# Optimization experiments

Hardware: AMD Instinct MI355X
Metric: run time of the kernel (lower is better)

The kernel has to match this reference:

```python
import jax, jax.numpy as jnp
import numpy as np

N, E, G = 50000, 800000, 16
H, C = 4, 64  # heads, per-head channels
NEG_SLOPE = 0.2

def gat_conv(x, src, dst, W, att_s, att_d, bias, heads, out_c, concat):
    # x: [N, Fin]; W: [Fin, heads*out_c]; att_s/att_d: [heads, out_c]
    h = (x @ W).reshape(N, heads, out_c)
    a_s = (h * att_s).sum(-1)              # [N, heads]
    a_d = (h * att_d).sum(-1)
    e = a_s[src] + a_d[dst]                # [E, heads]
    e = jnp.where(e >= 0, e, NEG_SLOPE * e)  # leaky_relu
    m = jax.ops.segment_max(e, dst, num_segments=N)
    ex = jnp.exp(e - m[dst])
    den = jax.ops.segment_sum(ex, dst, num_segments=N)
    alpha = ex / (den[dst] + 1e-16)        # segment softmax over incoming edges
    msg = h[src] * alpha[:, :, None]       # [E, heads, out_c]
    out = jax.ops.segment_sum(msg, dst, num_segments=N)
    out = out.reshape(N, heads * out_c) if concat else out.mean(axis=1)
    return out + bias

def setup_inputs() -> dict:
    key = jax.random.key(0)
    ks = jax.random.split(key, 30)
    def g(k, shape, scale=0.05):
        return (jax.random.normal(k, shape, dtype=jnp.float32) * scale)
    inp = {}
    inp['x'] = jax.random.normal(ks[0], (N, 32), dtype=jnp.float32)
    inp['edge_index'] = jax.random.randint(ks[1], (2, E), 0, N, dtype=jnp.int32)
    inp['batch'] = jnp.sort(jax.random.randint(ks[2], (N,), 0, G, dtype=jnp.int32))
    inp['global_features'] = jax.random.normal(ks[3], (G, 4), dtype=jnp.float32)
    # node encoder
    inp['W_enc'] = g(ks[4], (32, C)); inp['b_enc'] = g(ks[5], (C,))
    # conv1: 64 -> 4x64 concat
    inp['W1'] = g(ks[6], (C, H * C)); inp['as1'] = g(ks[7], (H, C)); inp['ad1'] = g(ks[8], (H, C)); inp['b1'] = g(ks[9], (H * C,))
    # conv2: 256 -> 4x64 concat
    inp['W2'] = g(ks[10], (H * C, H * C)); inp['as2'] = g(ks[11], (H, C)); inp['ad2'] = g(ks[12], (H, C)); inp['b2'] = g(ks[13], (H * C,))
    # conv3: 256 -> 1x64 no concat
    inp['W3'] = g(ks[14], (H * C, C)); inp['as3'] = g(ks[15], (1, C)); inp['ad3'] = g(ks[16], (1, C)); inp['b3'] = g(ks[17], (C,))
    # global processor
    inp['Wg'] = g(ks[18], (4, C)); inp['bg'] = g(ks[19], (C,))
    # decoder
    inp['Wd1'] = g(ks[20], (2 * C, C)); inp['bd1'] = g(ks[21], (C,))
    inp['gamma'] = jnp.ones((C,), jnp.float32); inp['beta'] = jnp.zeros((C,), jnp.float32)
    inp['Wd2'] = g(ks[22], (C, 256)); inp['bd2'] = g(ks[23], (256,))
    return inp

def reference(x, edge_index, batch, global_features, W_enc, b_enc,
              W1, as1, ad1, b1, W2, as2, ad2, b2, W3, as3, ad3, b3,
              Wg, bg, Wd1, bd1, gamma, beta, Wd2, bd2):
    # add self-loops (PyG GATConv default)
    loops = jnp.arange(N, dtype=edge_index.dtype)
    src = jnp.concatenate([edge_index[0], loops])
    dst = jnp.concatenate([edge_index[1], loops])
    h = x @ W_enc + b_enc
    h = gat_conv(h, src, dst, W1, as1, ad1, b1, H, C, True)
    h = jax.nn.elu(h)  # dropout is identity in eval
    h = gat_conv(h, src, dst, W2, as2, ad2, b2, H, C, True)
    h = jax.nn.elu(h)
    h = gat_conv(h, src, dst, W3, as3, ad3, b3, 1, C, False)
    # global mean pool per graph
    sums = jax.ops.segment_sum(h, batch, num_segments=G)
    cnts = jax.ops.segment_sum(jnp.ones((N, 1), h.dtype), batch, num_segments=G)
    pooled = sums / jnp.maximum(cnts, 1.0)
    genc = jax.nn.relu(global_features @ Wg + bg)
    z = jnp.concatenate([pooled, genc], axis=1)
    z = z @ Wd1 + bd1
    z = z * gamma + beta  # BatchNorm1d in eval mode (running stats 0/1)
    z = jax.nn.relu(z)
    out = z @ Wd2 + bd2
    return jax.nn.softmax(out, axis=1)
```

## Files before the change

kernel.cpp:

```cpp
#include <hip/hip_runtime.h>
#include <math.h>

#define NEG_SLOPE 0.2f
#define LOG2E 1.4426950408889634f

typedef __attribute__((ext_vector_type(8))) short short8;
typedef __attribute__((ext_vector_type(4))) float f32x4;

__device__ inline float b2f(unsigned short u) {
    union { unsigned int i; float f; } x; x.i = ((unsigned int)u) << 16; return x.f;
}
__device__ inline float b2f_lo(unsigned int u) {
    union { unsigned int i; float f; } x; x.i = u << 16; return x.f;
}
__device__ inline float b2f_hi(unsigned int u) {
    union { unsigned int i; float f; } x; x.i = u & 0xFFFF0000u; return x.f;
}
__device__ inline unsigned short f2b(float f) {
    union { float f; unsigned int i; } u; u.f = f;
    unsigned int r = u.i + 0x7FFF + ((u.i >> 16) & 1);
    return (unsigned short)(r >> 16);
}

__global__ void prep_kernel(const float* __restrict__ W1, const float* __restrict__ W2,
                            const float* __restrict__ W3, const float* __restrict__ as1,
                            const float* __restrict__ ad1,
                            unsigned short* __restrict__ Wt1, unsigned short* __restrict__ Wt2,
                            unsigned short* __restrict__ Wt3,
                            float* __restrict__ u1s, float* __restrict__ u1d,
                            int* __restrict__ counts, float* __restrict__ pooledP,
                            float* __restrict__ cntP, int N, int G, int zc) {
    const int b = blockIdx.x;
    const int t = threadIdx.x;
    if (b < 64) {
        int i = b * 256 + t;
        int k = i >> 8, m = i & 255;
        Wt1[(size_t)m * 64 + k] = f2b(W1[i]);
    } else if (b < 320) {
        int i = (b - 64) * 256 + t;
        int k = i >> 8, m = i & 255;
        Wt2[(size_t)m * 256 + k] = f2b(W2[i]);
    } else if (b < 384) {
        int i = (b - 320) * 256 + t;
        int k = i >> 6, m = i & 63;
        Wt3[(size_t)m * 256 + k] = f2b(W3[i]);
    } else if (b == 384) {
        int k = t >> 2, h = t & 3;
        float s = 0.0f, d = 0.0f;
        for (int c = 0; c < 64; c++) {
            float w = W1[k * 256 + h * 64 + c];
            s += w * as1[h * 64 + c];
            d += w * ad1[h * 64 + c];
        }
        u1s[k * 4 + h] = s;
        u1d[k * 4 + h] = d;
    } else if (b < 385 + zc) {
        int i = (b - 385) * 256 + t;
        if (i < N) counts[i] = 0;
    } else {
        int i = (b - 385 - zc) * 256 + t;
        if (i < 64 * G * 64) pooledP[i] = 0.0f;
        if (i < 64 * G) cntP[i] = 0.0f;
    }
}

__global__ __launch_bounds__(256) void gemm_enc(const float* __restrict__ A,
                                                const float* __restrict__ B,
                                                const float* __restrict__ bias,
                                                unsigned short* __restrict__ C16,
                                                const float* __restrict__ u1s,
                                                const float* __restrict__ u1d,
                                                float* __restrict__ a_s,
                                                float* __restrict__ a_d,
                                                int Nrows, int K, int M) {
    __shared__ float sA[16][64];
    __shared__ float sB[16][64];
    const int tx = threadIdx.x & 15;
    const int ty = threadIdx.x >> 4;
    const int row0 = blockIdx.x * 64;
    const int lr = threadIdx.x >> 2;
    const int lk = (threadIdx.x & 3) << 2;
    const int br = threadIdx.x >> 4;
    const int bc = (threadIdx.x & 15) << 2;

    const int aRow = row0 + lr;
    const bool aValid = aRow < Nrows;
    const float* Aptr = A + (size_t)aRow * K + lk;
    const float* Bptr = B + (size_t)br * M + bc;

    float acc[4][4] = {{0,0,0,0},{0,0,0,0},{0,0,0,0},{0,0,0,0}};
    float4 a = aValid ? *(const float4*)Aptr : float4{0,0,0,0};
    float4 b = *(const float4*)Bptr;

    for (int kt = 0; kt < K; kt += 16) {
        __syncthreads();
        sA[lk+0][lr] = a.x; sA[lk+1][lr] = a.y; sA[lk+2][lr] = a.z; sA[lk+3][lr] = a.w;
        *(float4*)&sB[br][bc] = b;
        __syncthreads();
        if (kt + 16 < K) {
            a = aValid ? *(const float4*)(Aptr + kt + 16) : float4{0,0,0,0};
            b = *(const float4*)(Bptr + (size_t)(kt + 16) * M);
        }
        #pragma unroll
        for (int k = 0; k < 16; k++) {
            const float4 av = *(const float4*)&sA[k][ty << 2];
            const float4 bv = *(const float4*)&sB[k][tx << 2];
            acc[0][0] += av.x*bv.x; acc[0][1] += av.x*bv.y; acc[0][2] += av.x*bv.z; acc[0][3] += av.x*bv.w;
            acc[1][0] += av.y*bv.x; acc[1][1] += av.y*bv.y; acc[1][2] += av.y*bv.z; acc[1][3] += av.y*bv.w;
            acc[2][0] += av.z*bv.x; acc[2][1] += av.z*bv.y; acc[2][2] += av.z*bv.z; acc[2][3] += av.z*bv.w;
            acc[3][0] += av.w*bv.x; acc[3][1] += av.w*bv.y; acc[3][2] += av.w*bv.z; acc[3][3] += av.w*bv.w;
        }
    }
    float4 bb = *(const float4*)&bias[tx << 2];
    #pragma unroll
    for (int i = 0; i < 4; i++) {
        acc[i][0] += bb.x; acc[i][1] += bb.y; acc[i][2] += bb.z; acc[i][3] += bb.w;
    }
    float4 us[4], ud[4];
    #pragma unroll
    for (int j = 0; j < 4; j++) {
        us[j] = *(const float4*)&u1s[((tx << 2) + j) * 4];
        ud[j] = *(const float4*)&u1d[((tx << 2) + j) * 4];
    }
    #pragma unroll
    for (int i = 0; i < 4; i++) {
        float4 ps = {0,0,0,0}, pd = {0,0,0,0};
        #pragma unroll
        for (int j = 0; j < 4; j++) {
            ps.x += acc[i][j] * us[j].x; ps.y += acc[i][j] * us[j].y;
            ps.z += acc[i][j] * us[j].z; ps.w += acc[i][j] * us[j].w;
            pd.x += acc[i][j] * ud[j].x; pd.y += acc[i][j] * ud[j].y;
            pd.z += acc[i][j] * ud[j].z; pd.w += acc[i][j] * ud[j].w;
        }
        #pragma unroll
        for (int off = 1; off < 16; off <<= 1) {
            ps.x += __shfl_xor(ps.x, off); ps.y += __shfl_xor(ps.y, off);
            ps.z += __shfl_xor(ps.z, off); ps.w += __shfl_xor(ps.w, off);
            pd.x += __shfl_xor(pd.x, off); pd.y += __shfl_xor(pd.y, off);
            pd.z += __shfl_xor(pd.z, off); pd.w += __shfl_xor(pd.w, off);
        }
        int r = row0 + (ty << 2) + i;
        if (tx == 0 && r < Nrows) {
            float4 o1 = {ps.x * LOG2E, ps.y * LOG2E, ps.z * LOG2E, ps.w * LOG2E};
            float4 o2 = {pd.x * LOG2E, pd.y * LOG2E, pd.z * LOG2E, pd.w * LOG2E};
            *(float4*)&a_s[r * 4] = o1;
            *(float4*)&a_d[r * 4] = o2;
        }
    }
    #pragma unroll
    for (int i = 0; i < 4; i++) {
        int r = row0 + (ty << 2) + i;
        if (r < Nrows) {
            ushort4 o = {f2b(acc[i][0]), f2b(acc[i][1]), f2b(acc[i][2]), f2b(acc[i][3])};
            *(ushort4*)&C16[(size_t)r * M + (tx << 2)] = o;
        }
    }
}

template<int CPW, int SCORES>
__global__ __launch_bounds__(256) void gemm_mfma(const unsigned short* __restrict__ A16,
                                                 const unsigned short* __restrict__ Bt16,
                                                 unsigned short* __restrict__ C16,
                                                 const float* __restrict__ att_s,
                                                 const float* __restrict__ att_d,
                                                 float* __restrict__ a_s,
                                                 float* __restrict__ a_d,
                                                 int Nrows, int K, int M, int H) {
    constexpr int BN = CPW * 64;
    __shared__ unsigned short sA[64][40];
    __shared__ unsigned short sB[BN][40];
    const int tid = threadIdx.x;
    const int wave = tid >> 6;
    const int lane = tid & 63;
    const int quad = lane >> 4;
    const int l16 = lane & 15;
    const int row0 = blockIdx.x * 64;
    const int col0 = blockIdx.y * BN;
    const int sr = tid >> 2;
    const int sk = (tid & 3) << 3;

    f32x4 acc[4][CPW];
    #pragma unroll
    for (int i = 0; i < 4; i++)
        #pragma unroll
        for (int j = 0; j < CPW; j++) acc[i][j] = (f32x4){0,0,0,0};

    for (int kt = 0; kt < K; kt += 32) {
        __syncthreads();
// ... 52 lines not shown
            if (l16 == 0) {
                #pragma unroll
                for (int r = 0; r < 4; r++) {
                    atomicAdd(&sSD[i * 16 + quad * 4 + r][hib][0], ps[r]);
                    atomicAdd(&sSD[i * 16 + quad * 4 + r][hib][1], pd[r]);
                }
            }
        }
        __syncthreads();
        for (int t = tid; t < 64 * CPW; t += 256) {
            int row = t & 63, hb = t >> 6;
            int r = row0 + row;
            if (r < Nrows) {
                int hg = (col0 >> 6) + hb;
                a_s[r * H + hg] = sSD[row][hb][0] * LOG2E;
                a_d[r * H + hg] = sSD[row][hb][1] * LOG2E;
            }
        }
    }
    #pragma unroll
    for (int i = 0; i < 4; i++) {
        #pragma unroll
        for (int j = 0; j < CPW; j++) {
            int col = col0 + wave * (CPW * 16) + j * 16 + l16;
            #pragma unroll
            for (int r = 0; r < 4; r++) {
                int row = row0 + i * 16 + quad * 4 + r;
                if (row < Nrows) C16[(size_t)row * M + col] = f2b(acc[i][j][r]);
            }
        }
    }
}

__global__ __launch_bounds__(256) void gemm_bd64(const unsigned short* __restrict__ A16,
                                                 const unsigned short* __restrict__ Bt16,
                                                 const float* __restrict__ bias,
                                                 unsigned short* __restrict__ C16,
                                                 int Nrows) {
    __shared__ unsigned short sA[64][40];
    __shared__ unsigned short sB[64][40];
    const int tid = threadIdx.x;
    const int wave = tid >> 6;
    const int lane = tid & 63;
    const int quad = lane >> 4;
    const int l16 = lane & 15;
    const int h = blockIdx.y;
    const int row0 = blockIdx.x * 64;
    const int sr = tid >> 2;
    const int sk = (tid & 3) << 3;

    f32x4 acc[4];
    #pragma unroll
    for (int i = 0; i < 4; i++) acc[i] = (f32x4){0,0,0,0};

    #pragma unroll
    for (int kt = 0; kt < 64; kt += 32) {
        __syncthreads();
        {
            int r = row0 + sr;
            uint4 z = {0,0,0,0};
            *(uint4*)&sA[sr][sk] = (r < Nrows)
                ? *(const uint4*)&A16[(size_t)r * 256 + h * 64 + kt + sk] : z;
        }
        *(uint4*)&sB[sr][sk] = *(const uint4*)&Bt16[(size_t)(h * 64 + sr) * 64 + kt + sk];
        __syncthreads();
        short8 bf = *(const short8*)&sB[wave * 16 + l16][quad * 8];
        #pragma unroll
        for (int i = 0; i < 4; i++) {
            short8 af = *(const short8*)&sA[i * 16 + l16][quad * 8];
            acc[i] = __builtin_amdgcn_mfma_f32_16x16x32_bf16(af, bf, acc[i], 0, 0, 0);
        }
    }
    const int col = h * 64 + wave * 16 + l16;
    const float bb = bias[col];
    #pragma unroll
    for (int i = 0; i < 4; i++) {
        #pragma unroll
        for (int r = 0; r < 4; r++) {
            int row = row0 + i * 16 + quad * 4 + r;
            if (row < Nrows) {
                float v = acc[i][r] + bb;
                v = (v > 0.0f) ? v : expm1f(v);
                C16[(size_t)row * 256 + col] = f2b(v);
            }
        }
    }
}

__global__ void edge_hist_kernel(const int* __restrict__ ei, int* __restrict__ counts,
                                 int E, int Et) {
    int e = blockIdx.x * 256 + threadIdx.x;
    if (e >= Et) return;
    int d = (e < E) ? ei[E + e] : e - E;
    atomicAdd(&counts[d], 1);
}

__global__ __launch_bounds__(1024) void scan_blocks(int* __restrict__ counts,
                                                    int* __restrict__ blockSums, int N) {
    __shared__ int wsum[16];
    const int tid = threadIdx.x;
    const int lane = tid & 63;
    const int wave = tid >> 6;
    int i = blockIdx.x * 1024 + tid;
    int v = (i < N) ? counts[i] : 0;
// ... 26 lines not shown
                          int N, int Et) {
    __shared__ int sbs[64];
    if (threadIdx.x < 64) {
        int lane = threadIdx.x;
        int v = (lane < nb) ? blockSums[lane] : 0;
        int s = v;
        #pragma unroll
        for (int off = 1; off < 64; off <<= 1) {
            int t = __shfl_up(s, off);
            if (lane >= off) s += t;
        }
        sbs[lane] = s - v;
    }
    __syncthreads();
    int i = blockIdx.x * 256 + threadIdx.x;
    if (i < N) {
        int o = excl[i] + sbs[i >> 10];
        offsets[i] = o;
        cursor[i] = o;
    }
    if (i == N) offsets[N] = Et;
}

__global__ void edge_sort_kernel(const int* __restrict__ ei, int* __restrict__ cursor,
                                 int* __restrict__ srcS, int E, int Et) {
    int e = blockIdx.x * 256 + threadIdx.x;
    if (e >= Et) return;
    int s, d;
    if (e < E) { s = ei[e]; d = ei[E + e]; } else { s = d = e - E; }
    int pos = atomicAdd(&cursor[d], 1);
    srcS[pos] = s;
}

__global__ __launch_bounds__(256) void gat_agg_in64(
        const int* __restrict__ offsets, const int* __restrict__ srcS,
        const float4* __restrict__ a_s4, const float4* __restrict__ a_d4,
        const unsigned short* __restrict__ h16,
        unsigned short* __restrict__ out16,
        int N) {
    __shared__ float wlds[4][64][4];
    __shared__ int slds[4][64];
    const int wid = threadIdx.x >> 6;
    const int n = blockIdx.x * 4 + wid;
    if (n >= N) return;
    const int lane = threadIdx.x & 63;
    const int half = lane >> 5;
    const int l32 = lane & 31;
    const int start = offsets[n], end = offsets[n + 1];
    const float4 ad = a_d4[n];
    float2 acc[4] = {{0,0},{0,0},{0,0},{0,0}};
    float4 den = {0,0,0,0};
    const int loff = l32 << 1;

    for (int e0 = start; e0 < end; e0 += 64) {
        const int cnt = min(64, end - e0);
        if (lane < cnt) {
            int sB = srcS[e0 + lane];
            slds[wid][lane] = sB;
            const float4 as = a_s4[sB];
            float x0 = as.x + ad.x; x0 = fmaxf(x0, NEG_SLOPE * x0);
            float x1 = as.y + ad.y; x1 = fmaxf(x1, NEG_SLOPE * x1);
            float x2 = as.z + ad.z; x2 = fmaxf(x2, NEG_SLOPE * x2);
            float x3 = as.w + ad.w; x3 = fmaxf(x3, NEG_SLOPE * x3);
            wlds[wid][lane][0] = exp2f(x0);
            wlds[wid][lane][1] = exp2f(x1);
            wlds[wid][lane][2] = exp2f(x2);
            wlds[wid][lane][3] = exp2f(x3);
        }
        int j = half;
        for (; j + 8 <= cnt + half; j += 8) {
            int ss[4]; float4 ww[4]; unsigned int gg[4];
            #pragma unroll
            for (int u = 0; u < 4; u++) {
                ss[u] = slds[wid][j + 2 * u];
                ww[u] = *(const float4*)&wlds[wid][j + 2 * u][0];
            }
            #pragma unroll
            for (int u = 0; u < 4; u++)
                gg[u] = *(const unsigned int*)&h16[((size_t)ss[u] << 6) + loff];
            #pragma unroll
            for (int u = 0; u < 4; u++) {
                const float vl = b2f_lo(gg[u]), vh = b2f_hi(gg[u]);
                acc[0].x += ww[u].x * vl; acc[0].y += ww[u].x * vh;
                acc[1].x += ww[u].y * vl; acc[1].y += ww[u].y * vh;
                acc[2].x += ww[u].z * vl; acc[2].y += ww[u].z * vh;
                acc[3].x += ww[u].w * vl; acc[3].y += ww[u].w * vh;
                den.x += ww[u].x; den.y += ww[u].y; den.z += ww[u].z; den.w += ww[u].w;
            }
        }
        for (; j < cnt; j += 2) {
            const int s = slds[wid][j];
            const float4 w = *(const float4*)&wlds[wid][j][0];
            const unsigned int g = *(const unsigned int*)&h16[((size_t)s << 6) + loff];
            const float vl = b2f_lo(g), vh = b2f_hi(g);
            acc[0].x += w.x * vl; acc[0].y += w.x * vh;
            acc[1].x += w.y * vl; acc[1].y += w.y * vh;
            acc[2].x += w.z * vl; acc[2].y += w.z * vh;
            acc[3].x += w.w * vl; acc[3].y += w.w * vh;
            den.x += w.x; den.y += w.y; den.z += w.z; den.w += w.w;
        }
    }
    #pragma unroll
    for (int h = 0; h < 4; h++) {
        acc[h].x += __shfl_xor(acc[h].x, 32);
        acc[h].y += __shfl_xor(acc[h].y, 32);
    }
    den.x += __shfl_xor(den.x, 32); den.y += __shfl_xor(den.y, 32);
    den.z += __shfl_xor(den.z, 32); den.w += __shfl_xor(den.w, 32);
    if (half == 0) {
        const float i0 = 1.0f / (den.x + 1e-16f);
        const float i1 = 1.0f / (den.y + 1e-16f);
        const float i2 = 1.0f / (den.z + 1e-16f);
        const float i3 = 1.0f / (den.w + 1e-16f);
        unsigned int o0 = (unsigned int)f2b(acc[0].x * i0) | ((unsigned int)f2b(acc[0].y * i0) << 16);
        unsigned int o1 = (unsigned int)f2b(acc[1].x * i1) | ((unsigned int)f2b(acc[1].y * i1) << 16);
        unsigned int o2 = (unsigned int)f2b(acc[2].x * i2) | ((unsigned int)f2b(acc[2].y * i2) << 16);
        unsigned int o3 = (unsigned int)f2b(acc[3].x * i3) | ((unsigned int)f2b(acc[3].y * i3) << 16);
        *(unsigned int*)&out16[(size_t)n * 256 + 0 * 64 + loff] = o0;
        *(unsigned int*)&out16[(size_t)n * 256 + 1 * 64 + loff] = o1;
        *(unsigned int*)&out16[(size_t)n * 256 + 2 * 64 + loff] = o2;
        *(unsigned int*)&out16[(size_t)n * 256 + 3 * 64 + loff] = o3;
    }
}

__global__ __launch_bounds__(256) void gat_fused4(
        const int* __restrict__ offsets, const int* __restrict__ srcS,
        const float4* __restrict__ a_s4, const float4* __restrict__ a_d4,
        const unsigned short* __restrict__ hW16, const float* __restrict__ bias,
        unsigned short* __restrict__ out16, int N) {
    __shared__ float wlds[4][64][4];
    __shared__ int slds[4][64];
    const int wid = threadIdx.x >> 6;
    const int n = blockIdx.x * 4 + wid;
    if (n >= N) return;
    const int lane = threadIdx.x & 63;
    const int quad = lane >> 4;
    const int start = offsets[n], end = offsets[n + 1];
    const float4 ad = a_d4[n];
    float4 acc = {0, 0, 0, 0};
    float den = 0.0f;
    const int loff = lane << 2;

    for (int e0 = start; e0 < end; e0 += 64) {
        const int cnt = min(64, end - e0);
        if (lane < cnt) {
            int sB = srcS[e0 + lane];
            slds[wid][lane] = sB;
            const float4 as = a_s4[sB];
            float x0 = as.x + ad.x; x0 = fmaxf(x0, NEG_SLOPE * x0);
            float x1 = as.y + ad.y; x1 = fmaxf(x1, NEG_SLOPE * x1);
            float x2 = as.z + ad.z; x2 = fmaxf(x2, NEG_SLOPE * x2);
            float x3 = as.w + ad.w; x3 = fmaxf(x3, NEG_SLOPE * x3);
            wlds[wid][lane][0] = exp2f(x0);
            wlds[wid][lane][1] = exp2f(x1);
            wlds[wid][lane][2] = exp2f(x2);
            wlds[wid][lane][3] = exp2f(x3);
        }
        int j = 0;
        for (; j + 4 <= cnt; j += 4) {
            const int s0 = __builtin_amdgcn_readfirstlane(slds[wid][j + 0]);
            const int s1 = __builtin_amdgcn_readfirstlane(slds[wid][j + 1]);
            const int s2 = __builtin_amdgcn_readfirstlane(slds[wid][j + 2]);
            const int s3 = __builtin_amdgcn_readfirstlane(slds[wid][j + 3]);
            const float w0 = wlds[wid][j + 0][quad];
            const float w1 = wlds[wid][j + 1][quad];
            const float w2 = wlds[wid][j + 2][quad];
            const float w3 = wlds[wid][j + 3][quad];
            const uint2 h0 = *(const uint2*)&hW16[((size_t)s0 << 8) + loff];
            const uint2 h1 = *(const uint2*)&hW16[((size_t)s1 << 8) + loff];
            const uint2 h2 = *(const uint2*)&hW16[((size_t)s2 << 8) + loff];
            const uint2 h3 = *(const uint2*)&hW16[((size_t)s3 << 8) + loff];
            acc.x += w0 * b2f_lo(h0.x); acc.y += w0 * b2f_hi(h0.x);
            acc.z += w0 * b2f_lo(h0.y); acc.w += w0 * b2f_hi(h0.y);
            acc.x += w1 * b2f_lo(h1.x); acc.y += w1 * b2f_hi(h1.x);
            acc.z += w1 * b2f_lo(h1.y); acc.w += w1 * b2f_hi(h1.y);
            acc.x += w2 * b2f_lo(h2.x); acc.y += w2 * b2f_hi(h2.x);
            acc.z += w2 * b2f_lo(h2.y); acc.w += w2 * b2f_hi(h2.y);
            acc.x += w3 * b2f_lo(h3.x); acc.y += w3 * b2f_hi(h3.x);
            acc.z += w3 * b2f_lo(h3.y); acc.w += w3 * b2f_hi(h3.y);
            den += (w0 + w1) + (w2 + w3);
        }
        for (; j < cnt; j++) {
            const int s = __builtin_amdgcn_readfirstlane(slds[wid][j]);
            const float w = wlds[wid][j][quad];
            const uint2 hv = *(const uint2*)&hW16[((size_t)s << 8) + loff];
            acc.x += w * b2f_lo(hv.x); acc.y += w * b2f_hi(hv.x);
            acc.z += w * b2f_lo(hv.y); acc.w += w * b2f_hi(hv.y);
            den += w;
        }
    }

    const float inv = 1.0f / (den + 1e-16f);
    const float4 bb = *(const float4*)&bias[loff];
    float v0 = acc.x * inv + bb.x; v0 = (v0 > 0.0f) ? v0 : expm1f(v0);
    float v1 = acc.y * inv + bb.y; v1 = (v1 > 0.0f) ? v1 : expm1f(v1);
    float v2 = acc.z * inv + bb.z; v2 = (v2 > 0.0f) ? v2 : expm1f(v2);
    float v3 = acc.w * inv + bb.w; v3 = (v3 > 0.0f) ? v3 : expm1f(v3);
    uint2 o;
    o.x = (unsigned int)f2b(v0) | ((unsigned int)f2b(v1) << 16);
    o.y = (unsigned int)f2b(v2) | ((unsigned int)f2b(v3) << 16);
    *(uint2*)&out16[(size_t)n * 256 + loff] = o;
}

__global__ __launch_bounds__(256) void gat_fused1(
        const int* __restrict__ offsets, const int* __restrict__ srcS,
        const float* __restrict__ a_s, const float* __restrict__ a_d,
        const unsigned short* __restrict__ hW16, const float* __restrict__ bias,
        const int* __restrict__ batch,
        float* __restrict__ pooledP, float* __restrict__ cntP, int N, int G) {
    __shared__ float wlds[4][64];
    __shared__ int slds[4][64];
    __shared__ float2 sOut[4][32];
    __shared__ int sG[4];
    const int wid = threadIdx.x >> 6;
    const int n = blockIdx.x * 4 + wid;
    const bool valid = n < N;
    const int lane = threadIdx.x & 63;
    const int half = lane >> 5;
    const int l32 = lane & 31;
    const int start = valid ? offsets[n] : 0;
    const int end   = valid ? offsets[n + 1] : 0;
    const float ad  = valid ? a_d[n] : 0.0f;
    float accx = 0.0f, accy = 0.0f, den = 0.0f;
    const int loff = l32 << 1;

    for (int e0 = start; e0 < end; e0 += 64) {
        const int cnt_ = min(64, end - e0);
        if (lane < cnt_) {
            int sB = srcS[e0 + lane];
            slds[wid][lane] = sB;
            float ev = a_s[sB] + ad;
            ev = fmaxf(ev, NEG_SLOPE * ev);
            wlds[wid][lane] = exp2f(ev);
        }
// ... 144 lines not shown
    const int*   batch = (const int*)  d_in[2];
    const float* gf    = (const float*)d_in[3];
    const float* W_enc = (const float*)d_in[4];
    const float* b_enc = (const float*)d_in[5];
    const float* W1  = (const float*)d_in[6];
    const float* as1 = (const float*)d_in[7];
    const float* ad1 = (const float*)d_in[8];
    const float* b1  = (const float*)d_in[9];
    const float* W2  = (const float*)d_in[10];
    const float* as2 = (const float*)d_in[11];
    const float* ad2 = (const float*)d_in[12];
    const float* b2  = (const float*)d_in[13];
    const float* W3  = (const float*)d_in[14];
    const float* as3 = (const float*)d_in[15];
    const float* ad3 = (const float*)d_in[16];
    const float* b3  = (const float*)d_in[17];
    const float* Wg  = (const float*)d_in[18];
    const float* bg  = (const float*)d_in[19];
    const float* Wd1 = (const float*)d_in[20];
    const float* bd1 = (const float*)d_in[21];
    const float* gm  = (const float*)d_in[22];
    const float* bt  = (const float*)d_in[23];
    const float* Wd2 = (const float*)d_in[24];
    const float* bd2 = (const float*)d_in[25];

    const int N  = in_sizes[2];
    const int E  = in_sizes[1] / 2;
    const int G  = in_sizes[3] / 4;
    const int Et = E + N;

    unsigned short* h16a = (unsigned short*)d_ws;
    unsigned short* h16b = h16a + (size_t)N * 256;
    unsigned short* h1_16 = h16b + (size_t)N * 256;
    unsigned short* Wt1  = h1_16 + (size_t)N * 64;
    unsigned short* Wt2  = Wt1 + 256 * 64;
    unsigned short* Wt3  = Wt2 + 256 * 256;
    float* a_s    = (float*)(Wt3 + 64 * 256);
    float* a_d    = a_s + (size_t)N * 4;
    float* u1s    = a_d + (size_t)N * 4;
    float* u1d    = u1s + 256;
    float* pooledP = u1d + 256;
    float* cntP   = pooledP + (size_t)64 * G * 64;
    int*   offsets = (int*)(cntP + 64 * G);
    int*   srcS    = offsets + (N + 1);
    int*   counts  = srcS + Et;
    int*   cursor  = counts + N;
    int*   blockSums = cursor + N;

    dim3 blk(256);
    auto cdiv = [](int a, int b) { return (a + b - 1) / b; };
    const int eBlocks = cdiv(Et, 256);
    const int rowBlocks = cdiv(N, 64);
    const int nScanBlocks = cdiv(N, 1024);
    const int zc = cdiv(N, 256);
    const int z2 = cdiv(64 * G * 64, 256);

    prep_kernel<<<385 + zc + z2, blk, 0, stream>>>(W1, W2, W3, as1, ad1, Wt1, Wt2, Wt3,
                                                   u1s, u1d, counts, pooledP, cntP, N, G, zc);
    edge_hist_kernel<<<eBlocks, blk, 0, stream>>>(ei, counts, E, Et);
    scan_blocks<<<nScanBlocks, 1024, 0, stream>>>(counts, blockSums, N);
    scan_add2<<<cdiv(N + 1, 256), blk, 0, stream>>>(counts, blockSums, nScanBlocks,
                                                    offsets, cursor, N, Et);
    edge_sort_kernel<<<eBlocks, blk, 0, stream>>>(ei, cursor, srcS, E, Et);

    gemm_enc<<<dim3(rowBlocks, 1), blk, 0, stream>>>(x, W_enc, b_enc, h1_16,
                                                     u1s, u1d, a_s, a_d, N, 32, 64);

    gat_agg_in64<<<cdiv(N, 4), blk, 0, stream>>>(offsets, srcS, (const float4*)a_s,
                                                 (const float4*)a_d, h1_16, h16a, N);
    gemm_bd64<<<dim3(rowBlocks, 4), blk, 0, stream>>>(h16a, Wt1, b1, h16b, N);

    gemm_mfma<2, 1><<<dim3(rowBlocks, 2), blk, 0, stream>>>(h16b, Wt2, h16a,
                                                            as2, ad2, a_s, a_d, N, 256, 256, 4);
    gat_fused4<<<cdiv(N, 4), blk, 0, stream>>>(offsets, srcS, (const float4*)a_s,
                                               (const float4*)a_d, h16a, b2, h16b, N);

    gemm_mfma<1, 1><<<dim3(rowBlocks, 1), blk, 0, stream>>>(h16b, Wt3, h1_16,
                                                            as3, ad3, a_s, a_d, N, 256, 64, 1);
    gat_fused1<<<cdiv(N, 4), blk, 0, stream>>>(offsets, srcS, a_s, a_d, h1_16, b3,
                                               batch, pooledP, cntP, N, G);

    final_kernel<<<G, blk, 0, stream>>>(pooledP, cntP, gf, Wg, bg, Wd1, bd1, gm, bt, Wd2, bd2,
                                        (float*)d_out, G);
}
```

Before: 429.6 us.

## Split layer-2 GAT aggregation across heads via grid y dimension

The 4-head aggregation kernel now launches one wave per (node, head) using a second grid dimension. Each wave handles a single 64-channel head slice, with two half-waves processing alternating edges and combining results by a cross-lane shuffle. This raises parallelism and memory-level concurrency for the gather. The cost is that srcS and a_s are re-read and exp weights recomputed once per head, and each gather is narrower (4 bytes per lane instead of 8).

```diff
diff --git a/kernel.cpp b/kernel.cpp
--- a/kernel.cpp
+++ b/kernel.cpp
@@ -493,83 +493,78 @@
     }
 }
 
-__global__ __launch_bounds__(256) void gat_fused4(
+__global__ __launch_bounds__(256) void gat_fused4h(
         const int* __restrict__ offsets, const int* __restrict__ srcS,
-        const float4* __restrict__ a_s4, const float4* __restrict__ a_d4,
-        const unsigned short* __restrict__ hW16, const float* __restrict__ bias,
-        unsigned short* __restrict__ out16, int N) {
-    __shared__ float wlds[4][64][4];
+        const float* __restrict__ a_s,
+        const float* __restrict__ a_d,
+        const unsigned short* __restrict__ hW16,
+        const float* __restrict__ bias,
+        unsigned short* __restrict__ out16,
+        int N) {
+    __shared__ float wlds[4][64];
     __shared__ int slds[4][64];
     const int wid = threadIdx.x >> 6;
     const int n = blockIdx.x * 4 + wid;
     if (n >= N) return;
+    const int h = blockIdx.y;
     const int lane = threadIdx.x & 63;
-    const int quad = lane >> 4;
+    const int half = lane >> 5;
+    const int l32 = lane & 31;
     const int start = offsets[n], end = offsets[n + 1];
-    const float4 ad = a_d4[n];
-    float4 acc = {0, 0, 0, 0};
-    float den = 0.0f;
-    const int loff = lane << 2;
+    const float ad = a_d[n * 4 + h];
+    float accx = 0.0f, accy = 0.0f, den = 0.0f;
+    const int loff = l32 << 1;
+    const size_t colbase = (size_t)h * 64 + loff;
 
     for (int e0 = start; e0 < end; e0 += 64) {
-        const int cnt = min(64, end - e0);
-        if (lane < cnt) {
+        const int cnt_ = min(64, end - e0);
+        if (lane < cnt_) {
             int sB = srcS[e0 + lane];
             slds[wid][lane] = sB;
-            const float4 as = a_s4[sB];
-            float x0 = as.x + ad.x; x0 = fmaxf(x0, NEG_SLOPE * x0);
-            float x1 = as.y + ad.y; x1 = fmaxf(x1, NEG_SLOPE * x1);
-            float x2 = as.z + ad.z; x2 = fmaxf(x2, NEG_SLOPE * x2);
-            float x3 = as.w + ad.w; x3 = fmaxf(x3, NEG_SLOPE * x3);
-            wlds[wid][lane][0] = exp2f(x0);
-            wlds[wid][lane][1] = exp2f(x1);
-            wlds[wid][lane][2] = exp2f(x2);
-            wlds[wid][lane][3] = exp2f(x3);
-        }
-        int j = 0;
-        for (; j + 4 <= cnt; j += 4) {
-            const int s0 = __builtin_amdgcn_readfirstlane(slds[wid][j + 0]);
-            const int s1 = __builtin_amdgcn_readfirstlane(slds[wid][j + 1]);
-            const int s2 = __builtin_amdgcn_readfirstlane(slds[wid][j + 2]);
-            const int s3 = __builtin_amdgcn_readfirstlane(slds[wid][j + 3]);
-            const float w0 = wlds[wid][j + 0][quad];
-            const float w1 = wlds[wid][j + 1][quad];
-            const float w2 = wlds[wid][j + 2][quad];
-            const float w3 = wlds[wid][j + 3][quad];
-            const uint2 h0 = *(const uint2*)&hW16[((size_t)s0 << 8) + loff];
-            const uint2 h1 = *(const uint2*)&hW16[((size_t)s1 << 8) + loff];
-            const uint2 h2 = *(const uint2*)&hW16[((size_t)s2 << 8) + loff];
-            const uint2 h3 = *(const uint2*)&hW16[((size_t)s3 << 8) + loff];
-            acc.x += w0 * b2f_lo(h0.x); acc.y += w0 * b2f_hi(h0.x);
-            acc.z += w0 * b2f_lo(h0.y); acc.w += w0 * b2f_hi(h0.y);
-            acc.x += w1 * b2f_lo(h1.x); acc.y += w1 * b2f_hi(h1.x);
-            acc.z += w1 * b2f_lo(h1.y); acc.w += w1 * b2f_hi(h1.y);
-            acc.x += w2 * b2f_lo(h2.x); acc.y += w2 * b2f_hi(h2.x);
-            acc.z += w2 * b2f_lo(h2.y); acc.w += w2 * b2f_hi(h2.y);
-            acc.x += w3 * b2f_lo(h3.x); acc.y += w3 * b2f_hi(h3.x);
-            acc.z += w3 * b2f_lo(h3.y); acc.w += w3 * b2f_hi(h3.y);
+            float ev = a_s[sB * 4 + h] + ad;
+            ev = fmaxf(ev, NEG_SLOPE * ev);
+            wlds[wid][lane] = exp2f(ev);
+        }
+        int j = half;
+        for (; j + 8 <= cnt_ + half; j += 8) {
+            const int s0 = slds[wid][j + 0];
+            const int s1 = slds[wid][j + 2];
+            const int s2 = slds[wid][j + 4];
+            const int s3 = slds[wid][j + 6];
+            const float w0 = wlds[wid][j + 0];
+            const float w1 = wlds[wid][j + 2];
+            const float w2 = wlds[wid][j + 4];
+            const float w3 = wlds[wid][j + 6];
+            const unsigned int h0 = *(const unsigned int*)&hW16[((size_t)s0 << 8) + colbase];
+            const unsigned int h1 = *(const unsigned int*)&hW16[((size_t)s1 << 8) + colbase];
+            const unsigned int h2 = *(const unsigned int*)&hW16[((size_t)s2 << 8) + colbase];
+            const unsigned int h3 = *(const unsigned int*)&hW16[((size_t)s3 << 8) + colbase];
+            accx += w0 * b2f_lo(h0); accy += w0 * b2f_hi(h0);
+            accx += w1 * b2f_lo(h1); accy += w1 * b2f_hi(h1);
+            accx += w2 * b2f_lo(h2); accy += w2 * b2f_hi(h2);
+            accx += w3 * b2f_lo(h3); accy += w3 * b2f_hi(h3);
             den += (w0 + w1) + (w2 + w3);
         }
-        for (; j < cnt; j++) {
-            const int s = __builtin_amdgcn_readfirstlane(slds[wid][j]);
-            const float w = wlds[wid][j][quad];
-            const uint2 hv = *(const uint2*)&hW16[((size_t)s << 8) + loff];
-            acc.x += w * b2f_lo(hv.x); acc.y += w * b2f_hi(hv.x);
-            acc.z += w * b2f_lo(hv.y); acc.w += w * b2f_hi(hv.y);
+        for (; j < cnt_; j += 2) {
+            const int s = slds[wid][j];
+            const float w = wlds[wid][j];
+            const unsigned int hv = *(const unsigned int*)&hW16[((size_t)s << 8) + colbase];
+            accx += w * b2f_lo(hv);
+            accy += w * b2f_hi(hv);
             den += w;
         }
     }
-
-    const float inv = 1.0f / (den + 1e-16f);
-    const float4 bb = *(const float4*)&bias[loff];
-    float v0 = acc.x * inv + bb.x; v0 = (v0 > 0.0f) ? v0 : expm1f(v0);
-    float v1 = acc.y * inv + bb.y; v1 = (v1 > 0.0f) ? v1 : expm1f(v1);
-    float v2 = acc.z * inv + bb.z; v2 = (v2 > 0.0f) ? v2 : expm1f(v2);
-    float v3 = acc.w * inv + bb.w; v3 = (v3 > 0.0f) ? v3 : expm1f(v3);
-    uint2 o;
-    o.x = (unsigned int)f2b(v0) | ((unsigned int)f2b(v1) << 16);
-    o.y = (unsigned int)f2b(v2) | ((unsigned int)f2b(v3) << 16);
-    *(uint2*)&out16[(size_t)n * 256 + loff] = o;
+    accx += __shfl_xor(accx, 32);
+    accy += __shfl_xor(accy, 32);
+    den  += __shfl_xor(den, 32);
+    if (half == 0) {
+        const float inv = 1.0f / (den + 1e-16f);
+        const float2 bb = *(const float2*)&bias[h * 64 + loff];
+        float v0 = accx * inv + bb.x; v0 = (v0 > 0.0f) ? v0 : expm1f(v0);
+        float v1 = accy * inv + bb.y; v1 = (v1 > 0.0f) ? v1 : expm1f(v1);
+        unsigned int o = (unsigned int)f2b(v0) | ((unsigned int)f2b(v1) << 16);
+        *(unsigned int*)&out16[(size_t)n * 256 + h * 64 + loff] = o;
+    }
 }
 
 __global__ __launch_bounds__(256) void gat_fused1(
@@ -820,8 +815,8 @@
 
     gemm_mfma<2, 1><<<dim3(rowBlocks, 2), blk, 0, stream>>>(h16b, Wt2, h16a,
                                                             as2, ad2, a_s, a_d, N, 256, 256, 4);
-    gat_fused4<<<cdiv(N, 4), blk, 0, stream>>>(offsets, srcS, (const float4*)a_s,
-                                               (const float4*)a_d, h16a, b2, h16b, N);
+    gat_fused4h<<<dim3(cdiv(N, 4), 4), blk, 0, stream>>>(offsets, srcS, a_s, a_d,
+                                                         h16a, b2, h16b, N);
 
     gemm_mfma<1, 1><<<dim3(rowBlocks, 1), blk, 0, stream>>>(h16b, Wt3, h1_16,
                                                             as3, ad3, a_s, a_d, N, 256, 64, 1);
```

Result: slower. 461.8 us (+7.5%).

## Fold encoder linear into conv1 weights and aggregate raw 32-dim inputs

Applied to the files above, without the earlier changes.

Because the node encoder is linear, W_enc is folded into W1 (and b_enc into the bias), and attention scores are computed directly from x. Conv1 then aggregates the raw 32-channel bf16 input features per head instead of the 64-channel encoded features, and the per-head GEMM after aggregation uses K=32 instead of 64. This halves the gather bytes in the first aggregation and drops the encoder GEMM, at the cost of an extra 128-wide per-node intermediate and some extra bf16 rounding of the pre-combined weights.

```diff
diff --git a/kernel.cpp b/kernel.cpp
--- a/kernel.cpp
+++ b/kernel.cpp
@@ -7,9 +7,6 @@
 typedef __attribute__((ext_vector_type(8))) short short8;
 typedef __attribute__((ext_vector_type(4))) float f32x4;
 
-__device__ inline float b2f(unsigned short u) {
-    union { unsigned int i; float f; } x; x.i = ((unsigned int)u) << 16; return x.f;
-}
 __device__ inline float b2f_lo(unsigned int u) {
     union { unsigned int i; float f; } x; x.i = u << 16; return x.f;
 }
@@ -22,29 +19,29 @@
     return (unsigned short)(r >> 16);
 }
 
-__global__ void prep_kernel(const float* __restrict__ W1, const float* __restrict__ W2,
+__global__ void prep_kernel(const float* __restrict__ W_enc, const float* __restrict__ b_enc,
+                            const float* __restrict__ W1, const float* __restrict__ W2,
                             const float* __restrict__ W3, const float* __restrict__ as1,
-                            const float* __restrict__ ad1,
-                            unsigned short* __restrict__ Wt1, unsigned short* __restrict__ Wt2,
-                            unsigned short* __restrict__ Wt3,
+                            const float* __restrict__ ad1, const float* __restrict__ b1,
+                            unsigned short* __restrict__ Wc1t, float* __restrict__ bc1,
+                            unsigned short* __restrict__ Wt2, unsigned short* __restrict__ Wt3,
                             float* __restrict__ u1s, float* __restrict__ u1d,
                             int* __restrict__ counts, float* __restrict__ pooledP,
                             float* __restrict__ cntP, int N, int G, int zc) {
     const int b = blockIdx.x;
     const int t = threadIdx.x;
-    if (b < 64) {
+    if (b < 32) {
         int i = b * 256 + t;
-        int k = i >> 8, m = i & 255;
-        Wt1[(size_t)m * 64 + k] = f2b(W1[i]);
-    } else if (b < 320) {
-        int i = (b - 64) * 256 + t;
-        int k = i >> 8, m = i & 255;
-        Wt2[(size_t)m * 256 + k] = f2b(W2[i]);
-    } else if (b < 384) {
-        int i = (b - 320) * 256 + t;
-        int k = i >> 6, m = i & 63;
-        Wt3[(size_t)m * 256 + k] = f2b(W3[i]);
-    } else if (b == 384) {
+        int h = i >> 11, rem = i & 2047, o = rem >> 5, j = rem & 31;
+        float s = 0.0f;
+        for (int k = 0; k < 64; k++)
+            s += W_enc[j * 64 + k] * W1[k * 256 + h * 64 + o];
+        Wc1t[i] = f2b(s);
+    } else if (b == 32) {
+        float s = b1[t];
+        for (int k = 0; k < 64; k++) s += b_enc[k] * W1[k * 256 + t];
+        bc1[t] = s;
+    } else if (b == 33) {
         int k = t >> 2, h = t & 3;
         float s = 0.0f, d = 0.0f;
         for (int c = 0; c < 64; c++) {
@@ -54,106 +51,69 @@
         }
         u1s[k * 4 + h] = s;
         u1d[k * 4 + h] = d;
-    } else if (b < 385 + zc) {
-        int i = (b - 385) * 256 + t;
+    } else if (b < 34 + 256) {
+        int i = (b - 34) * 256 + t;
+        int k = i >> 8, m = i & 255;
+        Wt2[(size_t)m * 256 + k] = f2b(W2[i]);
+    } else if (b < 34 + 256 + 64) {
+        int i = (b - 290) * 256 + t;
+        int k = i >> 6, m = i & 63;
+        Wt3[(size_t)m * 256 + k] = f2b(W3[i]);
+    } else if (b < 354 + zc) {
+        int i = (b - 354) * 256 + t;
         if (i < N) counts[i] = 0;
     } else {
-        int i = (b - 385 - zc) * 256 + t;
+        int i = (b - 354 - zc) * 256 + t;
         if (i < 64 * G * 64) pooledP[i] = 0.0f;
         if (i < 64 * G) cntP[i] = 0.0f;
     }
 }
 
-__global__ __launch_bounds__(256) void gemm_enc(const float* __restrict__ A,
-                                                const float* __restrict__ B,
-                                                const float* __restrict__ bias,
-                                                unsigned short* __restrict__ C16,
-                                                const float* __restrict__ u1s,
-                                                const float* __restrict__ u1d,
-                                                float* __restrict__ a_s,
-                                                float* __restrict__ a_d,
-                                                int Nrows, int K, int M) {
-    __shared__ float sA[16][64];
-    __shared__ float sB[16][64];
-    const int tx = threadIdx.x & 15;
-    const int ty = threadIdx.x >> 4;
-    const int row0 = blockIdx.x * 64;
-    const int lr = threadIdx.x >> 2;
-    const int lk = (threadIdx.x & 3) << 2;
-    const int br = threadIdx.x >> 4;
-    const int bc = (threadIdx.x & 15) << 2;
-
-    const int aRow = row0 + lr;
-    const bool aValid = aRow < Nrows;
-    const float* Aptr = A + (size_t)aRow * K + lk;
-    const float* Bptr = B + (size_t)br * M + bc;
-
-    float acc[4][4] = {{0,0,0,0},{0,0,0,0},{0,0,0,0},{0,0,0,0}};
-    float4 a = aValid ? *(const float4*)Aptr : float4{0,0,0,0};
-    float4 b = *(const float4*)Bptr;
-
-    for (int kt = 0; kt < K; kt += 16) {
-        __syncthreads();
-        sA[lk+0][lr] = a.x; sA[lk+1][lr] = a.y; sA[lk+2][lr] = a.z; sA[lk+3][lr] = a.w;
-        *(float4*)&sB[br][bc] = b;
-        __syncthreads();
-        if (kt + 16 < K) {
-            a = aValid ? *(const float4*)(Aptr + kt + 16) : float4{0,0,0,0};
-            b = *(const float4*)(Bptr + (size_t)(kt + 16) * M);
-        }
-        #pragma unroll
-        for (int k = 0; k < 16; k++) {
-            const float4 av = *(const float4*)&sA[k][ty << 2];
-            const float4 bv = *(const float4*)&sB[k][tx << 2];
-            acc[0][0] += av.x*bv.x; acc[0][1] += av.x*bv.y; acc[0][2] += av.x*bv.z; acc[0][3] += av.x*bv.w;
-            acc[1][0] += av.y*bv.x; acc[1][1] += av.y*bv.y; acc[1][2] += av.y*bv.z; acc[1][3] += av.y*bv.w;
-            acc[2][0] += av.z*bv.x; acc[2][1] += av.z*bv.y; acc[2][2] += av.z*bv.z; acc[2][3] += av.z*bv.w;
-            acc[3][0] += av.w*bv.x; acc[3][1] += av.w*bv.y; acc[3][2] += av.w*bv.z; acc[3][3] += av.w*bv.w;
-        }
-    }
-    float4 bb = *(const float4*)&bias[tx << 2];
-    #pragma unroll
-    for (int i = 0; i < 4; i++) {
-        acc[i][0] += bb.x; acc[i][1] += bb.y; acc[i][2] += bb.z; acc[i][3] += bb.w;
-    }
-    float4 us[4], ud[4];
-    #pragma unroll
-    for (int j = 0; j < 4; j++) {
-        us[j] = *(const float4*)&u1s[((tx << 2) + j) * 4];
-        ud[j] = *(const float4*)&u1d[((tx << 2) + j) * 4];
-    }
-    #pragma unroll
-    for (int i = 0; i < 4; i++) {
-        float4 ps = {0,0,0,0}, pd = {0,0,0,0};
-        #pragma unroll
-        for (int j = 0; j < 4; j++) {
-            ps.x += acc[i][j] * us[j].x; ps.y += acc[i][j] * us[j].y;
-            ps.z += acc[i][j] * us[j].z; ps.w += acc[i][j] * us[j].w;
-            pd.x += acc[i][j] * ud[j].x; pd.y += acc[i][j] * ud[j].y;
-            pd.z += acc[i][j] * ud[j].z; pd.w += acc[i][j] * ud[j].w;
-        }
-        #pragma unroll
-        for (int off = 1; off < 16; off <<= 1) {
-            ps.x += __shfl_xor(ps.x, off); ps.y += __shfl_xor(ps.y, off);
-            ps.z += __shfl_xor(ps.z, off); ps.w += __shfl_xor(ps.w, off);
-            pd.x += __shfl_xor(pd.x, off); pd.y += __shfl_xor(pd.y, off);
-            pd.z += __shfl_xor(pd.z, off); pd.w += __shfl_xor(pd.w, off);
-        }
-        int r = row0 + (ty << 2) + i;
-        if (tx == 0 && r < Nrows) {
-            float4 o1 = {ps.x * LOG2E, ps.y * LOG2E, ps.z * LOG2E, ps.w * LOG2E};
-            float4 o2 = {pd.x * LOG2E, pd.y * LOG2E, pd.z * LOG2E, pd.w * LOG2E};
-            *(float4*)&a_s[r * 4] = o1;
-            *(float4*)&a_d[r * 4] = o2;
-        }
-    }
-    #pragma unroll
-    for (int i = 0; i < 4; i++) {
-        int r = row0 + (ty << 2) + i;
-        if (r < Nrows) {
-            ushort4 o = {f2b(acc[i][0]), f2b(acc[i][1]), f2b(acc[i][2]), f2b(acc[i][3])};
-            *(ushort4*)&C16[(size_t)r * M + (tx << 2)] = o;
-        }
+__global__ __launch_bounds__(256) void score_x(
+        const float* __restrict__ x, const float* __restrict__ W_enc,
+        const float* __restrict__ b_enc,
+        const float* __restrict__ u1s, const float* __restrict__ u1d,
+        unsigned short* __restrict__ x16, float* __restrict__ a_s,
+        float* __restrict__ a_d, int N) {
+    __shared__ float sUs[32][4], sUd[32][4], sC[8];
+    __shared__ float sX[32][33];
+    const int t = threadIdx.x;
+    if (t < 128) {
+        int j = t >> 2, h = t & 3;
+        float s = 0.0f, d = 0.0f;
+        for (int k = 0; k < 64; k++) {
+            float w = W_enc[j * 64 + k];
+            s += w * u1s[k * 4 + h];
+            d += w * u1d[k * 4 + h];
+        }
+        sUs[j][h] = s; sUd[j][h] = d;
+    } else if (t < 136) {
+        int hh = t - 128;
+        const float* u = (hh < 4) ? u1s : u1d;
+        int h = hh & 3;
+        float c = 0.0f;
+        for (int k = 0; k < 64; k++) c += b_enc[k] * u[k * 4 + h];
+        sC[hh] = c;
+    }
+    const int n0 = blockIdx.x * 32;
+    const int row = t >> 3, col = (t & 7) << 2;
+    float4 xv = {0, 0, 0, 0};
+    if (n0 + row < N) xv = *(const float4*)&x[(size_t)(n0 + row) * 32 + col];
+    sX[row][col + 0] = xv.x; sX[row][col + 1] = xv.y;
+    sX[row][col + 2] = xv.z; sX[row][col + 3] = xv.w;
+    __syncthreads();
+    const int ni = t >> 3, oi = t & 7, h = oi & 3;
+    const bool isS = oi < 4;
+    float acc = sC[oi];
+    #pragma unroll 8
+    for (int j = 0; j < 32; j++) acc += sX[ni][j] * (isS ? sUs[j][h] : sUd[j][h]);
+    if (n0 + ni < N) {
+        float* out = isS ? a_s : a_d;
+        out[(size_t)(n0 + ni) * 4 + h] = acc * LOG2E;
+    }
+    if (n0 + row < N) {
+        ushort4 o = {f2b(xv.x), f2b(xv.y), f2b(xv.z), f2b(xv.w)};
+        *(ushort4*)&x16[(size_t)(n0 + row) * 32 + col] = o;
     }
 }
 
@@ -272,7 +232,7 @@
     }
 }
 
-__global__ __launch_bounds__(256) void gemm_bd64(const unsigned short* __restrict__ A16,
+__global__ __launch_bounds__(256) void gemm_bd32(const unsigned short* __restrict__ A16,
                                                  const unsigned short* __restrict__ Bt16,
                                                  const float* __restrict__ bias,
                                                  unsigned short* __restrict__ C16,
@@ -289,27 +249,20 @@
     const int sr = tid >> 2;
     const int sk = (tid & 3) << 3;
 
+    {
+        int r = row0 + sr;
+        uint4 z = {0,0,0,0};
+        *(uint4*)&sA[sr][sk] = (r < Nrows)
+            ? *(const uint4*)&A16[(size_t)r * 128 + h * 32 + sk] : z;
+        *(uint4*)&sB[sr][sk] = *(const uint4*)&Bt16[(size_t)(h * 64 + sr) * 32 + sk];
+    }
+    __syncthreads();
+    short8 bf = *(const short8*)&sB[wave * 16 + l16][quad * 8];
     f32x4 acc[4];
     #pragma unroll
-    for (int i = 0; i < 4; i++) acc[i] = (f32x4){0,0,0,0};
-
-    #pragma unroll
-    for (int kt = 0; kt < 64; kt += 32) {
-        __syncthreads();
-        {
-            int r = row0 + sr;
-            uint4 z = {0,0,0,0};
-            *(uint4*)&sA[sr][sk] = (r < Nrows)
-                ? *(const uint4*)&A16[(size_t)r * 256 + h * 64 + kt + sk] : z;
-        }
-        *(uint4*)&sB[sr][sk] = *(const uint4*)&Bt16[(size_t)(h * 64 + sr) * 64 + kt + sk];
-        __syncthreads();
-        short8 bf = *(const short8*)&sB[wave * 16 + l16][quad * 8];
-        #pragma unroll
-        for (int i = 0; i < 4; i++) {
-            short8 af = *(const short8*)&sA[i * 16 + l16][quad * 8];
-            acc[i] = __builtin_amdgcn_mfma_f32_16x16x32_bf16(af, bf, acc[i], 0, 0, 0);
-        }
+    for (int i = 0; i < 4; i++) {
+        short8 af = *(const short8*)&sA[i * 16 + l16][quad * 8];
+        acc[i] = __builtin_amdgcn_mfma_f32_16x16x32_bf16(af, bf, (f32x4){0,0,0,0}, 0, 0, 0);
     }
     const int col = h * 64 + wave * 16 + l16;
     const float bb = bias[col];
@@ -402,25 +355,25 @@
     srcS[pos] = s;
 }
 
-__global__ __launch_bounds__(256) void gat_agg_in64(
+__global__ __launch_bounds__(256) void gat_agg_x32(
         const int* __restrict__ offsets, const int* __restrict__ srcS,
         const float4* __restrict__ a_s4, const float4* __restrict__ a_d4,
-        const unsigned short* __restrict__ h16,
-        unsigned short* __restrict__ out16,
+        const unsigned short* __restrict__ x16,
+        unsigned short* __restrict__ aggX,
         int N) {
-    __shared__ float wlds[4][64][4];
+    __shared__ float4 wlds[4][64];
     __shared__ int slds[4][64];
     const int wid = threadIdx.x >> 6;
     const int n = blockIdx.x * 4 + wid;
     if (n >= N) return;
     const int lane = threadIdx.x & 63;
-    const int half = lane >> 5;
-    const int l32 = lane & 31;
+    const int q = lane >> 4;
+    const int l16 = lane & 15;
     const int start = offsets[n], end = offsets[n + 1];
     const float4 ad = a_d4[n];
-    float2 acc[4] = {{0,0},{0,0},{0,0},{0,0}};
+    float2 acc0 = {0,0}, acc1 = {0,0}, acc2 = {0,0}, acc3 = {0,0};
     float4 den = {0,0,0,0};
-    const int loff = l32 << 1;
+    const int loff = l16 << 1;
 
     for (int e0 = start; e0 < end; e0 += 64) {
         const int cnt = min(64, end - e0);
@@ -432,64 +385,77 @@
             float x1 = as.y + ad.y; x1 = fmaxf(x1, NEG_SLOPE * x1);
             float x2 = as.z + ad.z; x2 = fmaxf(x2, NEG_SLOPE * x2);
             float x3 = as.w + ad.w; x3 = fmaxf(x3, NEG_SLOPE * x3);
-            wlds[wid][lane][0] = exp2f(x0);
-            wlds[wid][lane][1] = exp2f(x1);
-            wlds[wid][lane][2] = exp2f(x2);
-            wlds[wid][lane][3] = exp2f(x3);
-        }
-        int j = half;
-        for (; j + 8 <= cnt + half; j += 8) {
+            wlds[wid][lane] = (float4){exp2f(x0), exp2f(x1), exp2f(x2), exp2f(x3)};
+        }
+        int j = q;
+        for (; j + 12 < cnt; j += 16) {
             int ss[4]; float4 ww[4]; unsigned int gg[4];
             #pragma unroll
             for (int u = 0; u < 4; u++) {
-                ss[u] = slds[wid][j + 2 * u];
-                ww[u] = *(const float4*)&wlds[wid][j + 2 * u][0];
+                ss[u] = slds[wid][j + 4 * u];
+                ww[u] = wlds[wid][j + 4 * u];
             }
             #pragma unroll
             for (int u = 0; u < 4; u++)
-                gg[u] = *(const unsigned int*)&h16[((size_t)ss[u] << 6) + loff];
+                gg[u] = *(const unsigned int*)&x16[((size_t)ss[u] << 5) + loff];
             #pragma unroll
             for (int u = 0; u < 4; u++) {
                 const float vl = b2f_lo(gg[u]), vh = b2f_hi(gg[u]);
-                acc[0].x += ww[u].x * vl; acc[0].y += ww[u].x * vh;
-                acc[1].x += ww[u].y * vl; acc[1].y += ww[u].y * vh;
-                acc[2].x += ww[u].z * vl; acc[2].y += ww[u].z * vh;
-                acc[3].x += ww[u].w * vl; acc[3].y += ww[u].w * vh;
+                acc0.x += ww[u].x * vl; acc0.y += ww[u].x * vh;
+                acc1.x += ww[u].y * vl; acc1.y += ww[u].y * vh;
+                acc2.x += ww[u].z * vl; acc2.y += ww[u].z * vh;
+                acc3.x += ww[u].w * vl; acc3.y += ww[u].w * vh;
                 den.x += ww[u].x; den.y += ww[u].y; den.z += ww[u].z; den.w += ww[u].w;
             }
         }
-        for (; j < cnt; j += 2) {
+        for (; j + 4 < cnt; j += 8) {
+            const int s0 = slds[wid][j], s1 = slds[wid][j + 4];
+            const float4 w0 = wlds[wid][j], w1 = wlds[wid][j + 4];
+            const unsigned int g0 = *(const unsigned int*)&x16[((size_t)s0 << 5) + loff];
+            const unsigned int g1 = *(const unsigned int*)&x16[((size_t)s1 << 5) + loff];
+            const float vl0 = b2f_lo(g0), vh0 = b2f_hi(g0);
+            const float vl1 = b2f_lo(g1), vh1 = b2f_hi(g1);
+            acc0.x += w0.x * vl0 + w1.x * vl1; acc0.y += w0.x * vh0 + w1.x * vh1;
+            acc1.x += w0.y * vl0 + w1.y * vl1; acc1.y += w0.y * vh0 + w1.y * vh1;
+            acc2.x += w0.z * vl0 + w1.z * vl1; acc2.y += w0.z * vh0 + w1.z * vh1;
+            acc3.x += w0.w * vl0 + w1.w * vl1; acc3.y += w0.w * vh0 + w1.w * vh1;
+            den.x += w0.x + w1.x; den.y += w0.y + w1.y;
+            den.z += w0.z + w1.z; den.w += w0.w + w1.w;
+        }
+        for (; j < cnt; j += 4) {
             const int s = slds[wid][j];
-            const float4 w = *(const float4*)&wlds[wid][j][0];
-            const unsigned int g = *(const unsigned int*)&h16[((size_t)s << 6) + loff];
+            const float4 w = wlds[wid][j];
+            const unsigned int g = *(const unsigned int*)&x16[((size_t)s << 5) + loff];
             const float vl = b2f_lo(g), vh = b2f_hi(g);
-            acc[0].x += w.x * vl; acc[0].y += w.x * vh;
-            acc[1].x += w.y * vl; acc[1].y += w.y * vh;
-            acc[2].x += w.z * vl; acc[2].y += w.z * vh;
-            acc[3].x += w.w * vl; acc[3].y += w.w * vh;
+            acc0.x += w.x * vl; acc0.y += w.x * vh;
+            acc1.x += w.y * vl; acc1.y += w.y * vh;
+            acc2.x += w.z * vl; acc2.y += w.z * vh;
+            acc3.x += w.w * vl; acc3.y += w.w * vh;
             den.x += w.x; den.y += w.y; den.z += w.z; den.w += w.w;
         }
     }
     #pragma unroll
-    for (int h = 0; h < 4; h++) {
-        acc[h].x += __shfl_xor(acc[h].x, 32);
-        acc[h].y += __shfl_xor(acc[h].y, 32);
-    }
-    den.x += __shfl_xor(den.x, 32); den.y += __shfl_xor(den.y, 32);
-    den.z += __shfl_xor(den.z, 32); den.w += __shfl_xor(den.w, 32);
-    if (half == 0) {
+    for (int off = 16; off < 64; off <<= 1) {
+        acc0.x += __shfl_xor(acc0.x, off); acc0.y += __shfl_xor(acc0.y, off);
+        acc1.x += __shfl_xor(acc1.x, off); acc1.y += __shfl_xor(acc1.y, off);
+        acc2.x += __shfl_xor(acc2.x, off); acc2.y += __shfl_xor(acc2.y, off);
+        acc3.x += __shfl_xor(acc3.x, off); acc3.y += __shfl_xor(acc3.y, off);
+        den.x += __shfl_xor(den.x, off); den.y += __shfl_xor(den.y, off);
+        den.z += __shfl_xor(den.z, off); den.w += __shfl_xor(den.w, off);
+    }
+    if (q == 0) {
         const float i0 = 1.0f / (den.x + 1e-16f);
         const float i1 = 1.0f / (den.y + 1e-16f);
         const float i2 = 1.0f / (den.z + 1e-16f);
         const float i3 = 1.0f / (den.w + 1e-16f);
-        unsigned int o0 = (unsigned int)f2b(acc[0].x * i0) | ((unsigned int)f2b(acc[0].y * i0) << 16);
-        unsigned int o1 = (unsigned int)f2b(acc[1].x * i1) | ((unsigned int)f2b(acc[1].y * i1) << 16);
-        unsigned int o2 = (unsigned int)f2b(acc[2].x * i2) | ((unsigned int)f2b(acc[2].y * i2) << 16);
-        unsigned int o3 = (unsigned int)f2b(acc[3].x * i3) | ((unsigned int)f2b(acc[3].y * i3) << 16);
-        *(unsigned int*)&out16[(size_t)n * 256 + 0 * 64 + loff] = o0;
-        *(unsigned int*)&out16[(size_t)n * 256 + 1 * 64 + loff] = o1;
-        *(unsigned int*)&out16[(size_t)n * 256 + 2 * 64 + loff] = o2;
-        *(unsigned int*)&out16[(size_t)n * 256 + 3 * 64 + loff] = o3;
+        unsigned int o0 = (unsigned int)f2b(acc0.x * i0) | ((unsigned int)f2b(acc0.y * i0) << 16);
+        unsigned int o1 = (unsigned int)f2b(acc1.x * i1) | ((unsigned int)f2b(acc1.y * i1) << 16);
+        unsigned int o2 = (unsigned int)f2b(acc2.x * i2) | ((unsigned int)f2b(acc2.y * i2) << 16);
+        unsigned int o3 = (unsigned int)f2b(acc3.x * i3) | ((unsigned int)f2b(acc3.y * i3) << 16);
+        *(unsigned int*)&aggX[((size_t)n << 7) + 0 * 32 + loff] = o0;
+        *(unsigned int*)&aggX[((size_t)n << 7) + 1 * 32 + loff] = o1;
+        *(unsigned int*)&aggX[((size_t)n << 7) + 2 * 32 + loff] = o2;
+        *(unsigned int*)&aggX[((size_t)n << 7) + 3 * 32 + loff] = o3;
     }
 }
 
@@ -780,10 +746,12 @@
     unsigned short* h16a = (unsigned short*)d_ws;
     unsigned short* h16b = h16a + (size_t)N * 256;
     unsigned short* h1_16 = h16b + (size_t)N * 256;
-    unsigned short* Wt1  = h1_16 + (size_t)N * 64;
-    unsigned short* Wt2  = Wt1 + 256 * 64;
+    unsigned short* x16  = h1_16 + (size_t)N * 64;
+    unsigned short* Wc1t = x16 + (size_t)N * 32;
+    unsigned short* Wt2  = Wc1t + 4 * 64 * 32;
     unsigned short* Wt3  = Wt2 + 256 * 256;
-    float* a_s    = (float*)(Wt3 + 64 * 256);
+    float* bc1    = (float*)(Wt3 + 64 * 256);
+    float* a_s    = bc1 + 256;
     float* a_d    = a_s + (size_t)N * 4;
     float* u1s    = a_d + (size_t)N * 4;
     float* u1d    = u1s + 256;
@@ -803,20 +771,20 @@
     const int zc = cdiv(N, 256);
     const int z2 = cdiv(64 * G * 64, 256);
 
-    prep_kernel<<<385 + zc + z2, blk, 0, stream>>>(W1, W2, W3, as1, ad1, Wt1, Wt2, Wt3,
-                                                   u1s, u1d, counts, pooledP, cntP, N, G, zc);
+    prep_kernel<<<354 + zc + z2, blk, 0, stream>>>(W_enc, b_enc, W1, W2, W3, as1, ad1, b1,
+                                                   Wc1t, bc1, Wt2, Wt3, u1s, u1d,
+                                                   counts, pooledP, cntP, N, G, zc);
     edge_hist_kernel<<<eBlocks, blk, 0, stream>>>(ei, counts, E, Et);
     scan_blocks<<<nScanBlocks, 1024, 0, stream>>>(counts, blockSums, N);
     scan_add2<<<cdiv(N + 1, 256), blk, 0, stream>>>(counts, blockSums, nScanBlocks,
                                                     offsets, cursor, N, Et);
     edge_sort_kernel<<<eBlocks, blk, 0, stream>>>(ei, cursor, srcS, E, Et);
 
-    gemm_enc<<<dim3(rowBlocks, 1), blk, 0, stream>>>(x, W_enc, b_enc, h1_16,
-                                                     u1s, u1d, a_s, a_d, N, 32, 64);
-
-    gat_agg_in64<<<cdiv(N, 4), blk, 0, stream>>>(offsets, srcS, (const float4*)a_s,
-                                                 (const float4*)a_d, h1_16, h16a, N);
-    gemm_bd64<<<dim3(rowBlocks, 4), blk, 0, stream>>>(h16a, Wt1, b1, h16b, N);
+    score_x<<<cdiv(N, 32), blk, 0, stream>>>(x, W_enc, b_enc, u1s, u1d, x16, a_s, a_d, N);
+
+    gat_agg_x32<<<cdiv(N, 4), blk, 0, stream>>>(offsets, srcS, (const float4*)a_s,
+                                                (const float4*)a_d, x16, h16a, N);
+    gemm_bd32<<<dim3(rowBlocks, 4), blk, 0, stream>>>(h16a, Wc1t, bc1, h16b, N);
 
     gemm_mfma<2, 1><<<dim3(rowBlocks, 2), blk, 0, stream>>>(h16b, Wt2, h16a,
                                                             as2, ad2, a_s, a_d, N, 256, 256, 4);
```

Result: no change. 424.6 us (-1.2%).
